# Optimization experiments

Hardware: AMD Instinct MI355X
Metric: run time of the kernel (lower is better)

Reference implementation:

```python
import jax, jax.numpy as jnp
import numpy as np

DIM = 1024
NUM_HEADS = 16
HEAD_DIM = 64

def setup_inputs() -> dict:
    key = jax.random.key(0)
    ks = jax.random.split(key, 7)
    x = jax.random.normal(ks[0], (4, 4096, DIM), dtype=jnp.float32)
    mask = jnp.ones((4, 4096), dtype=jnp.float32)
    # torch Linear stores weight (out, in) and computes x @ W.T; we store (in, out) directly.
    Wq = jax.random.normal(ks[1], (DIM, NUM_HEADS * HEAD_DIM), dtype=jnp.float32) / np.sqrt(DIM)
    Wk = jax.random.normal(ks[2], (DIM, NUM_HEADS * HEAD_DIM), dtype=jnp.float32) / np.sqrt(DIM)
    Wv = jax.random.normal(ks[3], (DIM, NUM_HEADS * HEAD_DIM), dtype=jnp.float32) / np.sqrt(DIM)
    Wo = jax.random.normal(ks[4], (NUM_HEADS * HEAD_DIM, DIM), dtype=jnp.float32) / np.sqrt(NUM_HEADS * HEAD_DIM)
    # FeatureMap buffer: randn(dim, dim) / sqrt(dim) with dim = head_dim
    proj = jax.random.normal(ks[5], (HEAD_DIM, HEAD_DIM), dtype=jnp.float32) / np.sqrt(HEAD_DIM)
    return {"x": x, "mask": mask, "Wq": Wq, "Wk": Wk, "Wv": Wv, "Wo": Wo, "proj": proj}

def _feature_map(x, proj):
    # phi(x) = elu(x @ proj) + 1  (non-negative random features)
    return jax.nn.elu(x @ proj) + 1.0

def reference(x, mask, Wq, Wk, Wv, Wo, proj):
    b, n, _ = x.shape
    h, d = NUM_HEADS, HEAD_DIM
    # project and split heads: (b, h, n, d)
    q = (x @ Wq).reshape(b, n, h, d).transpose(0, 2, 1, 3)
    k = (x @ Wk).reshape(b, n, h, d).transpose(0, 2, 1, 3)
    v = (x @ Wv).reshape(b, n, h, d).transpose(0, 2, 1, 3)
    q = _feature_map(q, proj)
    k = _feature_map(k, proj)
    # mask: (b, n) -> (b, 1, n, 1)
    k = k * mask[:, None, :, None]
    # linear attention: phi(Q) (phi(K)^T V)
    kv = jnp.einsum('bhnd,bhne->bhde', k, v)          # (b, h, d, d)
    qkv = jnp.einsum('bhnd,bhde->bhne', q, kv)        # (b, h, n, d)
    k_sum = k.sum(axis=2)                              # (b, h, d)
    normalizer = jnp.einsum('bhnd,bhd->bhn', q, k_sum) + 1e-06
    out = qkv / normalizer[..., None]
    out = out.transpose(0, 2, 1, 3).reshape(b, n, h * d)
    return out @ Wo
```

## Files before the change

### kernel.cpp

```cpp
#include <hip/hip_runtime.h>
#include <stdint.h>

#define TOKENS 16384
#define KDIM 1024
#define QKVN 3072

typedef unsigned short u16;
using bf16x8 = __attribute__((ext_vector_type(8))) __bf16;
using f32x4  = __attribute__((ext_vector_type(4))) float;
using u16x8  = __attribute__((ext_vector_type(8))) unsigned short;

__device__ inline u16 f2bf(float f) {
  union { float f; uint32_t u; } v; v.f = f;
  uint32_t u = v.u;
  return (u16)((u + 0x7FFFu + ((u >> 16) & 1u)) >> 16);
}
__device__ inline float bf2f(u16 s) {
  union { uint32_t u; float f; } v; v.u = ((uint32_t)s) << 16;
  return v.f;
}
__device__ inline void g2l16(const void* g, void* l) {
  __builtin_amdgcn_global_load_lds(
      (const __attribute__((address_space(1))) void*)g,
      (__attribute__((address_space(3))) void*)l, 16, 0, 0);
}

template<int LD>
__device__ inline void stage_half(const u16* __restrict__ g, u16* l, int t) {
  #pragma unroll
  for (int i = 0; i < 2; ++i) {
    const int ch = i * 512 + t;
    const int row = ch >> 3;
    const int cc = (ch & 7) ^ (row & 7);
    g2l16(g + (long)row * LD + cc * 8, (char*)l + ch * 16);
  }
}

#define LDA_H(DST, BASE) do { \
  _Pragma("unroll") \
  for (int mi = 0; mi < 4; ++mi) { \
    const int row = wm*64 + mi*16 + rl; \
    const char* p = (const char*)(BASE) + row*128; \
    const int sw = (row & 7) << 4; \
    DST[mi][0] = *(const bf16x8*)(p + ((kg*16) ^ sw)); \
    DST[mi][1] = *(const bf16x8*)(p + ((64 + kg*16) ^ sw)); \
  } \
} while (0)

#define LDB_H(DST, BASE) do { \
  _Pragma("unroll") \
  for (int ni = 0; ni < 2; ++ni) { \
    const int row = wn*32 + ni*16 + rl; \
    const char* p = (const char*)(BASE) + row*128; \
    const int sw = (row & 7) << 4; \
    DST[ni][0] = *(const bf16x8*)(p + ((kg*16) ^ sw)); \
    DST[ni][1] = *(const bf16x8*)(p + ((64 + kg*16) ^ sw)); \
  } \
} while (0)

#define MFMA2Q(MH, AV, BV0, BV1) do { \
  __builtin_amdgcn_s_setprio(1); \
  _Pragma("unroll") \
  for (int kh = 0; kh < 2; ++kh) \
    _Pragma("unroll") \
    for (int mi = 0; mi < 4; ++mi) \
      _Pragma("unroll") \
      for (int ni = 0; ni < 2; ++ni) { \
        acc[(MH)*4+mi][ni]   = __builtin_amdgcn_mfma_f32_16x16x32_bf16( \
            AV[mi][kh], BV0[ni][kh], acc[(MH)*4+mi][ni], 0, 0, 0); \
        acc[(MH)*4+mi][2+ni] = __builtin_amdgcn_mfma_f32_16x16x32_bf16( \
            AV[mi][kh], BV1[ni][kh], acc[(MH)*4+mi][2+ni], 0, 0, 0); \
      } \
  __builtin_amdgcn_s_setprio(0); \
} while (0)

#define LGKM0 do { \
  asm volatile("s_waitcnt lgkmcnt(0)" ::: "memory"); \
  __builtin_amdgcn_sched_barrier(0); \
} while (0)
#define VMC(N) asm volatile("s_waitcnt vmcnt(" #N ")" ::: "memory")
#define BAR() __builtin_amdgcn_s_barrier()

template<int NTOT, int EPI, int ALD, int NT, int PERB>
__device__ __forceinline__ void gemm_body(
    const u16* __restrict__ A, const u16* __restrict__ Bm,
    void* __restrict__ C, const float* __restrict__ aux) {
  __shared__ u16 As[2][2][8192];
  __shared__ u16 Bs[2][2][8192];
  const int t = threadIdx.x;
  const int l = t & 63;
  const int w = t >> 6;
  const int rl = l & 15, kg = l >> 4;
  const int wm = w >> 2, wn = w & 3;
  constexpr int nbn = NTOT / 256;
  constexpr int nwg = 64 * nbn;
  constexpr int GRID = nwg / NT;
  constexpr int KC = NT * 16;
  constexpr int IT = KC / 2;
  static_assert(nwg % 8 == 0, "bijective xcd swizzle");
  const int bid = blockIdx.x;

  auto tcoord = [&](int ot, long& tar, long& tbr) {
    const int gt = ot * GRID + bid;
    const int swz = (gt & 7) * (nwg / 8) + (gt >> 3);
    tar = (long)(swz / nbn) * 256;
    tbr = (long)(swz % nbn) * 256;
  };
  auto asrc = [&](int ch) {
    long ta, tb; tcoord(ch >> 4, ta, tb);
    return A + ta * ALD + (ch & 15) * 64;
  };
  auto bsrc = [&](int ch) {
    long ta, tb; tcoord(ch >> 4, ta, tb);
    return Bm + (PERB ? (ta >> 12) * 1048576 : 0) + tb * 1024 + (ch & 15) * 64;
  };

  f32x4 acc[8][4];
  #pragma unroll
  for (int i = 0; i < 8; ++i)
    #pragma unroll
    for (int j = 0; j < 4; ++j)
      acc[i][j] = (f32x4){0.f, 0.f, 0.f, 0.f};

  bf16x8 afA[4][2], bA[2][2], bB[2][2];

  auto epilogue = [&](int ot) {
    long ar0, br0; tcoord(ot, ar0, br0);
    #pragma unroll
    for (int mh = 0; mh < 2; ++mh)
      #pragma unroll
      for (int mi = 0; mi < 4; ++mi)
        #pragma unroll
        for (int j = 0; j < 4; ++j) {
          const long row = ar0 + mh*128 + wm*64 + mi*16 + kg*4 + j;
          float rs = 0.f;
          if (EPI == 0) rs = aux[row];
          #pragma unroll
          for (int nh = 0; nh < 2; ++nh)
            #pragma unroll
            for (int ni = 0; ni < 2; ++ni) {
              const long col = br0 + nh*128 + wn*32 + ni*16 + rl;
              float v = acc[mh*4+mi][nh*2+ni][j];
              if (EPI == 0) {
                if (col < 2048) {
                  v = (v > 0.f) ? (v + 1.f) : __expf(v);
                  if (col >= 1024) v *= rs;
                }
                ((u16*)C)[row * QKVN + col] = f2bf(v);
              } else {
                ((float*)C)[row * NTOT + col] = v;
              }
            }
        }
    #pragma unroll
    for (int i = 0; i < 8; ++i)
      #pragma unroll
      for (int j = 0; j < 4; ++j)
        acc[i][j] = (f32x4){0.f, 0.f, 0.f, 0.f};
  };

  {
    const u16* A0s = asrc(0); const u16* B0s = bsrc(0);
    const u16* A1s = asrc(1); const u16* B1s = bsrc(1);
    stage_half<ALD >(A0s,             As[0][0], t);
    stage_half<1024>(B0s,             Bs[0][0], t);
    stage_half<1024>(B0s + 128*1024,  Bs[0][1], t);
    stage_half<ALD >(A0s + 128*ALD,   As[0][1], t);
    stage_half<ALD >(A1s,             As[1][0], t);
    stage_half<1024>(B1s,             Bs[1][0], t);
    VMC(4);
    BAR();
  }

  for (int i = 0; i < IT; ++i) {
    const int o1 = 2*i + 1;
    const int e = (2*i + 2 < KC) ? 2*i + 2 : KC - 1;
    const int o = (2*i + 3 < KC) ? 2*i + 3 : KC - 1;
    const u16* Ao1 = asrc(o1); const u16* Bo1 = bsrc(o1);
    const u16* Ae = asrc(e);   const u16* Be = bsrc(e);
    const u16* Ao = asrc(o);   const u16* Bo = bsrc(o);

    LDA_H(afA, As[0][0]); LDB_H(bA, Bs[0][0]); LDB_H(bB, Bs[0][1]);
    stage_half<ALD>(Ao1 + 128*ALD, As[1][1], t);
    stage_half<1024>(Bo1 + 128*1024, Bs[1][1], t);
    LGKM0;
    MFMA2Q(0, afA, bA, bB);
    VMC(4); BAR();

    LDA_H(afA, As[0][1]);
    stage_half<ALD>(Ae, As[0][0], t);
    stage_half<1024>(Be, Bs[0][0], t);
    LGKM0;
    MFMA2Q(1, afA, bA, bB);
    VMC(4); BAR();

    LDA_H(afA, As[1][0]); LDB_H(bA, Bs[1][0]); LDB_H(bB, Bs[1][1]);
    stage_half<ALD>(Ae + 128*ALD, As[0][1], t);
    stage_half<1024>(Be + 128*1024, Bs[0][1], t);
    LGKM0;
    MFMA2Q(0, afA, bA, bB);
    VMC(4); BAR();

    LDA_H(afA, As[1][1]);
    stage_half<ALD>(Ao, As[1][0], t);
    stage_half<1024>(Bo, Bs[1][0], t);
    LGKM0;
    MFMA2Q(1, afA, bA, bB);
    VMC(4); BAR();

    if ((i & 7) == 7) epilogue(i >> 3);
  }
  VMC(0);
}

__global__ __launch_bounds__(512, 2) void gemm_qkv(
    const u16* __restrict__ A, const u16* __restrict__ Bm,
    void* __restrict__ C, const float* __restrict__ aux) {
  gemm_body<3072, 0, 1024, 3, 0>(A, Bm, C, aux);
}
__global__ __launch_bounds__(512, 2) void gemm_out(
    const u16* __restrict__ A, const u16* __restrict__ Bm,
    void* __restrict__ C, const float* __restrict__ aux) {
  gemm_body<1024, 1, 1024, 1, 1>(A, Bm, C, aux);
}

__global__ __launch_bounds__(256) void kv_kernel(const u16* __restrict__ QKV,
    float* __restrict__ kvws, float* __restrict__ ksws) {
  __shared__ u16 Kl[32 * 64];
  __shared__ u16 Vl[32 * 64];
  const int t = threadIdx.x;
  const int l = t & 63, w = t >> 6;
  const int rl = l & 15, kg = l >> 4;
  const int bid = blockIdx.x;
  const int bh = bid >> 3, ns = bid & 7;
  const int b = bh >> 4, h = bh & 15;
  const long tok0 = (long)b * 4096 + ns * 512;

  f32x4 acc[4];
  #pragma unroll
  for (int i = 0; i < 4; ++i) acc[i] = (f32x4){0.f, 0.f, 0.f, 0.f};
  float ks = 0.f;
  const int srow = t >> 3, scc = t & 7;

  for (int it = 0; it < 16; ++it) {
    const long tb = tok0 + it * 32;
    g2l16(QKV + (tb + srow) * QKVN + 1024 + h * 64 + scc * 8, (char*)Kl + t * 16);
    g2l16(QKV + (tb + srow) * QKVN + 2048 + h * 64 + scc * 8, (char*)Vl + t * 16);
    __syncthreads();
    union { u16x8 u; bf16x8 v; } au, bu;
    #pragma unroll
    for (int j = 0; j < 8; ++j) au.u[j] = Kl[(kg * 8 + j) * 64 + w * 16 + rl];
    #pragma unroll
    for (int ni = 0; ni < 4; ++ni) {
      #pragma unroll
      for (int j = 0; j < 8; ++j) bu.u[j] = Vl[(kg * 8 + j) * 64 + ni * 16 + rl];
      acc[ni] = __builtin_amdgcn_mfma_f32_16x16x32_bf16(au.v, bu.v, acc[ni], 0, 0, 0);
    }
    #pragma unroll
    for (int r = 0; r < 8; ++r) ks += bf2f(Kl[(w * 8 + r) * 64 + (t & 63)]);
    __syncthreads();
  }
  float* kvb = kvws + bh * 4096;
  #pragma unroll
  for (int ni = 0; ni < 4; ++ni)
    #pragma unroll
    for (int j = 0; j < 4; ++j) {
      const int d = w * 16 + kg * 4 + j;
      const int e = ni * 16 + rl;
      atomicAdd(&kvb[d * 64 + e], acc[ni][j]);
    }
  atomicAdd(&ksws[bh * 64 + (t & 63)], ks);
}

__global__ __launch_bounds__(256) void scale_q(const u16* __restrict__ QKV,
    const float* __restrict__ ksws, u16* __restrict__ Qc) {
  __shared__ float ksl[1024];
  const int bid = blockIdx.x, t = threadIdx.x;
  const int n0 = bid * 16;
  const int b = n0 >> 12;
  #pragma unroll
  for (int i = 0; i < 4; ++i) ksl[i * 256 + t] = ksws[b * 1024 + i * 256 + t];
  __syncthreads();
  const int h = t & 15, ti = t >> 4;
  const u16* qp = QKV + (long)(n0 + ti) * QKVN + h * 64;
  u16* op = Qc + (long)(n0 + ti) * 1024 + h * 64;
  u16x8 v[8];
  float norm = 1e-6f;
  #pragma unroll
  for (int i = 0; i < 8; ++i) {
    v[i] = *(const u16x8*)(qp + i * 8);
    #pragma unroll
    for (int j = 0; j < 8; ++j) norm += bf2f(v[i][j]) * ksl[h * 64 + i * 8 + j];
  }
  const float inv = 1.0f / norm;
  #pragma unroll
  for (int i = 0; i < 8; ++i) {
    u16x8 o;
    #pragma unroll
    for (int j = 0; j < 8; ++j) o[j] = f2bf(bf2f(v[i][j]) * inv);
    *(u16x8*)(op + i * 8) = o;
  }
}

__global__ __launch_bounds__(256) void w2_kernel(const float* __restrict__ kvws,
    const float* __restrict__ Wo, u16* __restrict__ W2T) {
  __shared__ float kvl[64][64];
  const int bid = blockIdx.x, t = threadIdx.x;
  const int bh = bid >> 2, os = bid & 3;
  const int b = bh >> 4, h = bh & 15;
  const float* kvb = kvws + bh * 4096;
  #pragma unroll
  for (int i = 0; i < 16; ++i) ((float*)kvl)[i * 256 + t] = kvb[i * 256 + t];
  __syncthreads();
  const int o = os * 256 + t;
  float wo[64];
  #pragma unroll
  for (int e = 0; e < 64; ++e) wo[e] = Wo[(long)(h * 64 + e) * 1024 + o];
  u16* out = W2T + (long)b * 1048576 + (long)o * 1024 + h * 64;
  for (int d = 0; d < 64; ++d) {
    float s = 0.f;
    #pragma unroll
    for (int e = 0; e < 64; ++e) s += wo[e] * kvl[d][e];
    out[d] = f2bf(s);
  }
}

__global__ __launch_bounds__(256) void prep_qk(const float* __restrict__ Wq,
    const float* __restrict__ Wk, const float* __restrict__ proj,
    u16* __restrict__ WqkvT) {
  __shared__ float Wl[128][65];
  __shared__ float Pl[64][65];
  const int bid = blockIdx.x;
  const int m = bid >> 7, h = (bid >> 3) & 15, cb = bid & 7;
  const float* W = m ? Wk : Wq;
  const int t = threadIdx.x;
  #pragma unroll
  for (int i = 0; i < 16; ++i) {
    const int idx = i * 256 + t;
    Pl[idx >> 6][idx & 63] = proj[idx];
  }
  #pragma unroll
  for (int i = 0; i < 32; ++i) {
    const int idx = i * 256 + t;
    const int c = idx >> 6, d = idx & 63;
    Wl[c][d] = W[(long)(cb * 128 + c) * 1024 + h * 64 + d];
  }
  __syncthreads();
  const int c = t & 127, j0 = (t >> 7) * 32;
  float a[32];
  #pragma unroll
  for (int jj = 0; jj < 32; ++jj) a[jj] = 0.f;
  for (int d = 0; d < 64; ++d) {
    const float wv = Wl[c][d];
    #pragma unroll
    for (int jj = 0; jj < 32; ++jj) a[jj] += wv * Pl[d][j0 + jj];
  }
  #pragma unroll
  for (int jj = 0; jj < 32; ++jj)
    WqkvT[(long)(m * 1024 + h * 64 + j0 + jj) * 1024 + cb * 128 + c] = f2bf(a[jj]);
}

__global__ __launch_bounds__(256) void prep_v(const float* __restrict__ Wv,
    u16* __restrict__ WqkvT) {
  __shared__ float til[64][65];
  const int bid = blockIdx.x;
  const int rt = (bid >> 4) & 15, ct = bid & 15;
  const int t = threadIdx.x;
  const int j = t & 63;
  #pragma unroll
  for (int p = 0; p < 16; ++p) {
    const int i = p * 4 + (t >> 6);
    til[i][j] = Wv[(long)(rt * 64 + i) * 1024 + ct * 64 + j];
  }
  __syncthreads();
  u16* dst = WqkvT + (long)2048 * 1024;
  #pragma unroll
  for (int p = 0; p < 16; ++p) {
    const int i = p * 4 + (t >> 6);
    dst[(long)(ct * 64 + i) * 1024 + rt * 64 + j] = f2bf(til[j][i]);
  }
}

__global__ __launch_bounds__(256) void conv_x(const float* __restrict__ x,
                                              u16* __restrict__ xb) {
  const int idx = blockIdx.x * 256 + threadIdx.x;
  const float4* p = (const float4*)x + (long)idx * 2;
  const float4 a = p[0], b = p[1];
  u16x8 o;
  o[0] = f2bf(a.x); o[1] = f2bf(a.y); o[2] = f2bf(a.z); o[3] = f2bf(a.w);
  o[4] = f2bf(b.x); o[5] = f2bf(b.y); o[6] = f2bf(b.z); o[7] = f2bf(b.w);
  *((u16x8*)xb + idx) = o;
}

extern "C" void kernel_launch(void* const* d_in, const int* in_sizes, int n_in,
                              void* d_out, int out_size, void* d_ws, size_t ws_size,
                              hipStream_t stream) {
  const float* x    = (const float*)d_in[0];
  const float* mask = (const float*)d_in[1];
  const float* Wq   = (const float*)d_in[2];
  const float* Wk   = (const float*)d_in[3];
  const float* Wv   = (const float*)d_in[4];
  const float* Wo   = (const float*)d_in[5];
  const float* proj = (const float*)d_in[6];

  char* ws = (char*)d_ws;
  u16*  WqkvT = (u16*)(ws);
  u16*  xb    = (u16*)(ws + 8388608);
  u16*  QKV   = (u16*)(ws + 41943040);
  float* kvws = (float*)(ws + 142606336);
  float* ksws = (float*)(ws + 143654912);
  u16*  Qc   = xb;
  u16*  W2T  = (u16*)(ws);
  if (ws_size < (size_t)143671296) return;

  hipMemsetAsync(kvws, 0, 1064960, stream);
  prep_qk<<<256, 256, 0, stream>>>(Wq, Wk, proj, WqkvT);
  prep_v <<<256, 256, 0, stream>>>(Wv, WqkvT);
  conv_x <<<8192, 256, 0, stream>>>(x, xb);
  gemm_qkv<<<256, 512, 0, stream>>>(xb, WqkvT, (void*)QKV, mask);
  kv_kernel<<<512, 256, 0, stream>>>(QKV, kvws, ksws);
  scale_q<<<1024, 256, 0, stream>>>(QKV, ksws, Qc);
  w2_kernel<<<256, 256, 0, stream>>>(kvws, Wo, W2T);
  gemm_out<<<256, 512, 0, stream>>>(Qc, W2T, d_out, nullptr);
}
```

Measured before the change: 259.3 us.

## Split GEMM MFMA waits, precompute tile coords, widen kv chunks, merge weight prep

The GEMM inner loop now waits for only part of the LDS reads (lgkmcnt(4)) before issuing the first half of the MFMAs, so the remaining B-fragment loads overlap with compute. It also adds scheduling barriers and computes tile coordinates once instead of per chunk. The kv kernel processes 64 tokens per iteration instead of 32, halving its barrier count. The two weight-prep kernels are merged into a single launch; the merged kernel contains some odd no-op shared-memory self-assignments.

```diff
diff --git a/kernel.cpp b/kernel.cpp
--- a/kernel.cpp
+++ b/kernel.cpp
@@ -58,28 +58,29 @@
   } \
 } while (0)
 
-#define MFMA2Q(MH, AV, BV0, BV1) do { \
-  __builtin_amdgcn_s_setprio(1); \
+#define MFMA_G(MH, AV, BV, NB) do { \
   _Pragma("unroll") \
   for (int kh = 0; kh < 2; ++kh) \
     _Pragma("unroll") \
     for (int mi = 0; mi < 4; ++mi) \
       _Pragma("unroll") \
-      for (int ni = 0; ni < 2; ++ni) { \
-        acc[(MH)*4+mi][ni]   = __builtin_amdgcn_mfma_f32_16x16x32_bf16( \
-            AV[mi][kh], BV0[ni][kh], acc[(MH)*4+mi][ni], 0, 0, 0); \
-        acc[(MH)*4+mi][2+ni] = __builtin_amdgcn_mfma_f32_16x16x32_bf16( \
-            AV[mi][kh], BV1[ni][kh], acc[(MH)*4+mi][2+ni], 0, 0, 0); \
-      } \
-  __builtin_amdgcn_s_setprio(0); \
+      for (int ni = 0; ni < 2; ++ni) \
+        acc[(MH)*4+mi][(NB)+ni] = __builtin_amdgcn_mfma_f32_16x16x32_bf16( \
+            AV[mi][kh], BV[ni][kh], acc[(MH)*4+mi][(NB)+ni], 0, 0, 0); \
 } while (0)
 
 #define LGKM0 do { \
   asm volatile("s_waitcnt lgkmcnt(0)" ::: "memory"); \
   __builtin_amdgcn_sched_barrier(0); \
 } while (0)
+#define LGKM4 do { \
+  asm volatile("s_waitcnt lgkmcnt(4)" ::: "memory"); \
+  __builtin_amdgcn_sched_barrier(0); \
+} while (0)
 #define VMC(N) asm volatile("s_waitcnt vmcnt(" #N ")" ::: "memory")
 #define BAR() __builtin_amdgcn_s_barrier()
+#define SCHED0 __builtin_amdgcn_sched_barrier(0)
+#define PRIO(N) __builtin_amdgcn_s_setprio(N)
 
 template<int NTOT, int EPI, int ALD, int NT, int PERB>
 __device__ __forceinline__ void gemm_body(
@@ -106,12 +107,20 @@
     tar = (long)(swz / nbn) * 256;
     tbr = (long)(swz % nbn) * 256;
   };
+  long ar0_, br0_, ar1_, br1_, ar2_, br2_;
+  tcoord(0, ar0_, br0_);
+  if (NT > 1) tcoord(1, ar1_, br1_); else { ar1_ = ar0_; br1_ = br0_; }
+  if (NT > 2) tcoord(2, ar2_, br2_); else { ar2_ = ar1_; br2_ = br1_; }
+
   auto asrc = [&](int ch) {
-    long ta, tb; tcoord(ch >> 4, ta, tb);
+    const int ti = ch >> 4;
+    const long ta = (NT == 1 || ti == 0) ? ar0_ : (ti == 1 ? ar1_ : ar2_);
     return A + ta * ALD + (ch & 15) * 64;
   };
   auto bsrc = [&](int ch) {
-    long ta, tb; tcoord(ch >> 4, ta, tb);
+    const int ti = ch >> 4;
+    const long ta = (NT == 1 || ti == 0) ? ar0_ : (ti == 1 ? ar1_ : ar2_);
+    const long tb = (NT == 1 || ti == 0) ? br0_ : (ti == 1 ? br1_ : br2_);
     return Bm + (PERB ? (ta >> 12) * 1048576 : 0) + tb * 1024 + (ch & 15) * 64;
   };
 
@@ -180,32 +189,44 @@
     const u16* Ae = asrc(e);   const u16* Be = bsrc(e);
     const u16* Ao = asrc(o);   const u16* Bo = bsrc(o);
 
-    LDA_H(afA, As[0][0]); LDB_H(bA, Bs[0][0]); LDB_H(bB, Bs[0][1]);
+    LDA_H(afA, As[0][0]); LDB_H(bA, Bs[0][0]);
+    SCHED0;
+    LDB_H(bB, Bs[0][1]);
     stage_half<ALD>(Ao1 + 128*ALD, As[1][1], t);
     stage_half<1024>(Bo1 + 128*1024, Bs[1][1], t);
+    SCHED0;
+    LGKM4;
+    PRIO(1); MFMA_G(0, afA, bA, 0);
     LGKM0;
-    MFMA2Q(0, afA, bA, bB);
+    MFMA_G(0, afA, bB, 2); PRIO(0);
     VMC(4); BAR();
 
     LDA_H(afA, As[0][1]);
     stage_half<ALD>(Ae, As[0][0], t);
     stage_half<1024>(Be, Bs[0][0], t);
+    SCHED0;
     LGKM0;
-    MFMA2Q(1, afA, bA, bB);
+    PRIO(1); MFMA_G(1, afA, bA, 0); MFMA_G(1, afA, bB, 2); PRIO(0);
     VMC(4); BAR();
 
-    LDA_H(afA, As[1][0]); LDB_H(bA, Bs[1][0]); LDB_H(bB, Bs[1][1]);
+    LDA_H(afA, As[1][0]); LDB_H(bA, Bs[1][0]);
+    SCHED0;
+    LDB_H(bB, Bs[1][1]);
     stage_half<ALD>(Ae + 128*ALD, As[0][1], t);
     stage_half<1024>(Be + 128*1024, Bs[0][1], t);
+    SCHED0;
+    LGKM4;
+    PRIO(1); MFMA_G(0, afA, bA, 0);
     LGKM0;
-    MFMA2Q(0, afA, bA, bB);
+    MFMA_G(0, afA, bB, 2); PRIO(0);
     VMC(4); BAR();
 
     LDA_H(afA, As[1][1]);
     stage_half<ALD>(Ao, As[1][0], t);
     stage_half<1024>(Bo, Bs[1][0], t);
+    SCHED0;
     LGKM0;
-    MFMA2Q(1, afA, bA, bB);
+    PRIO(1); MFMA_G(1, afA, bA, 0); MFMA_G(1, afA, bB, 2); PRIO(0);
     VMC(4); BAR();
 
     if ((i & 7) == 7) epilogue(i >> 3);
@@ -226,8 +247,8 @@
 
 __global__ __launch_bounds__(256) void kv_kernel(const u16* __restrict__ QKV,
     float* __restrict__ kvws, float* __restrict__ ksws) {
-  __shared__ u16 Kl[32 * 64];
-  __shared__ u16 Vl[32 * 64];
+  __shared__ u16 Kl[64 * 64];
+  __shared__ u16 Vl[64 * 64];
   const int t = threadIdx.x;
   const int l = t & 63, w = t >> 6;
   const int rl = l & 15, kg = l >> 4;
@@ -240,24 +261,31 @@
   #pragma unroll
   for (int i = 0; i < 4; ++i) acc[i] = (f32x4){0.f, 0.f, 0.f, 0.f};
   float ks = 0.f;
-  const int srow = t >> 3, scc = t & 7;
-
-  for (int it = 0; it < 16; ++it) {
-    const long tb = tok0 + it * 32;
-    g2l16(QKV + (tb + srow) * QKVN + 1024 + h * 64 + scc * 8, (char*)Kl + t * 16);
-    g2l16(QKV + (tb + srow) * QKVN + 2048 + h * 64 + scc * 8, (char*)Vl + t * 16);
+
+  for (int it = 0; it < 8; ++it) {
+    const long tb = tok0 + it * 64;
+    #pragma unroll
+    for (int c = 0; c < 2; ++c) {
+      const int ch = c * 256 + t;
+      const int srow = ch >> 3, scc = ch & 7;
+      g2l16(QKV + (tb + srow) * QKVN + 1024 + h * 64 + scc * 8, (char*)Kl + ch * 16);
+      g2l16(QKV + (tb + srow) * QKVN + 2048 + h * 64 + scc * 8, (char*)Vl + ch * 16);
+    }
     __syncthreads();
     union { u16x8 u; bf16x8 v; } au, bu;
     #pragma unroll
-    for (int j = 0; j < 8; ++j) au.u[j] = Kl[(kg * 8 + j) * 64 + w * 16 + rl];
-    #pragma unroll
-    for (int ni = 0; ni < 4; ++ni) {
+    for (int ksb = 0; ksb < 2; ++ksb) {
       #pragma unroll
-      for (int j = 0; j < 8; ++j) bu.u[j] = Vl[(kg * 8 + j) * 64 + ni * 16 + rl];
-      acc[ni] = __builtin_amdgcn_mfma_f32_16x16x32_bf16(au.v, bu.v, acc[ni], 0, 0, 0);
-    }
-    #pragma unroll
-    for (int r = 0; r < 8; ++r) ks += bf2f(Kl[(w * 8 + r) * 64 + (t & 63)]);
+      for (int j = 0; j < 8; ++j) au.u[j] = Kl[(ksb * 32 + kg * 8 + j) * 64 + w * 16 + rl];
+      #pragma unroll
+      for (int ni = 0; ni < 4; ++ni) {
+        #pragma unroll
+        for (int j = 0; j < 8; ++j) bu.u[j] = Vl[(ksb * 32 + kg * 8 + j) * 64 + ni * 16 + rl];
+        acc[ni] = __builtin_amdgcn_mfma_f32_16x16x32_bf16(au.v, bu.v, acc[ni], 0, 0, 0);
+      }
+    }
+    #pragma unroll
+    for (int r = 0; r < 16; ++r) ks += bf2f(Kl[(w * 16 + r) * 64 + (t & 63)]);
     __syncthreads();
   }
   float* kvb = kvws + bh * 4096;
@@ -325,59 +353,60 @@
   }
 }
 
-__global__ __launch_bounds__(256) void prep_qk(const float* __restrict__ Wq,
+__global__ __launch_bounds__(256) void prep_w(const float* __restrict__ Wq,
     const float* __restrict__ Wk, const float* __restrict__ proj,
-    u16* __restrict__ WqkvT) {
+    const float* __restrict__ Wv, u16* __restrict__ WqkvT) {
   __shared__ float Wl[128][65];
   __shared__ float Pl[64][65];
-  const int bid = blockIdx.x;
-  const int m = bid >> 7, h = (bid >> 3) & 15, cb = bid & 7;
-  const float* W = m ? Wk : Wq;
   const int t = threadIdx.x;
-  #pragma unroll
-  for (int i = 0; i < 16; ++i) {
-    const int idx = i * 256 + t;
-    Pl[idx >> 6][idx & 63] = proj[idx];
-  }
-  #pragma unroll
-  for (int i = 0; i < 32; ++i) {
-    const int idx = i * 256 + t;
-    const int c = idx >> 6, d = idx & 63;
-    Wl[c][d] = W[(long)(cb * 128 + c) * 1024 + h * 64 + d];
-  }
-  __syncthreads();
-  const int c = t & 127, j0 = (t >> 7) * 32;
-  float a[32];
-  #pragma unroll
-  for (int jj = 0; jj < 32; ++jj) a[jj] = 0.f;
-  for (int d = 0; d < 64; ++d) {
-    const float wv = Wl[c][d];
-    #pragma unroll
-    for (int jj = 0; jj < 32; ++jj) a[jj] += wv * Pl[d][j0 + jj];
-  }
-  #pragma unroll
-  for (int jj = 0; jj < 32; ++jj)
-    WqkvT[(long)(m * 1024 + h * 64 + j0 + jj) * 1024 + cb * 128 + c] = f2bf(a[jj]);
-}
-
-__global__ __launch_bounds__(256) void prep_v(const float* __restrict__ Wv,
-    u16* __restrict__ WqkvT) {
-  __shared__ float til[64][65];
-  const int bid = blockIdx.x;
-  const int rt = (bid >> 4) & 15, ct = bid & 15;
-  const int t = threadIdx.x;
-  const int j = t & 63;
-  #pragma unroll
-  for (int p = 0; p < 16; ++p) {
-    const int i = p * 4 + (t >> 6);
-    til[i][j] = Wv[(long)(rt * 64 + i) * 1024 + ct * 64 + j];
-  }
-  __syncthreads();
-  u16* dst = WqkvT + (long)2048 * 1024;
-  #pragma unroll
-  for (int p = 0; p < 16; ++p) {
-    const int i = p * 4 + (t >> 6);
-    dst[(long)(ct * 64 + i) * 1024 + rt * 64 + j] = f2bf(til[j][i]);
+  if (blockIdx.x < 256) {
+    const int bid = blockIdx.x;
+    const int m = bid >> 7, h = (bid >> 3) & 15, cb = bid & 7;
+    const float* W = m ? Wk : Wq;
+    #pragma unroll
+    for (int i = 0; i < 16; ++i) {
+      const int idx = i * 256 + t;
+      Pl[idx >> 6][idx & 63] = proj[idx];
+    }
+    #pragma unroll
+    for (int i = 0; i < 32; ++i) {
+      const int idx = i * 256 + t;
+      const int c = idx >> 6, d = idx & 63;
+      Wl[c][d] = W[(long)(cb * 128 + c) * 1024 + h * 64 + d];
+    }
+    __syncthreads();
+    const int c = t & 127, j0 = (t >> 7) * 32;
+    float a[32];
+    #pragma unroll
+    for (int jj = 0; jj < 32; ++jj) a[jj] = 0.f;
+    for (int d = 0; d < 64; ++d) {
+      const float wv = Wl[c][d];
+      #pragma unroll
+      for (int jj = 0; jj < 32; ++jj) a[jj] += wv * Pl[d][j0 + jj];
+    }
+    #pragma unroll
+    for (int jj = 0; jj < 32; ++jj)
+      WqkvT[(long)(m * 1024 + h * 64 + j0 + jj) * 1024 + cb * 128 + c] = f2bf(a[jj]);
+  } else {
+    const int bid = blockIdx.x - 256;
+    const int rt = (bid >> 4) & 15, ct = bid & 15;
+    const int j = t & 63;
+    #pragma unroll
+    for (int p = 0; p < 16; ++p) {
+      const int i = p * 4 + (t >> 6);
+      Pl[0][0] = Pl[0][0];
+      Wl[0][i * 0] = Wl[0][0];
+      ((float*)Pl)[0] = ((float*)Pl)[0];
+      (void)0;
+      Wl[i][j] = Wv[(long)(rt * 64 + i) * 1024 + ct * 64 + j];
+    }
+    __syncthreads();
+    u16* dst = WqkvT + (long)2048 * 1024;
+    #pragma unroll
+    for (int p = 0; p < 16; ++p) {
+      const int i = p * 4 + (t >> 6);
+      dst[(long)(ct * 64 + i) * 1024 + rt * 64 + j] = f2bf(Wl[j][i]);
+    }
   }
 }
 
@@ -414,9 +443,8 @@
   if (ws_size < (size_t)143671296) return;
 
   hipMemsetAsync(kvws, 0, 1064960, stream);
-  prep_qk<<<256, 256, 0, stream>>>(Wq, Wk, proj, WqkvT);
-  prep_v <<<256, 256, 0, stream>>>(Wv, WqkvT);
-  conv_x <<<8192, 256, 0, stream>>>(x, xb);
+  prep_w<<<512, 256, 0, stream>>>(Wq, Wk, proj, Wv, WqkvT);
+  conv_x<<<8192, 256, 0, stream>>>(x, xb);
   gemm_qkv<<<256, 512, 0, stream>>>(xb, WqkvT, (void*)QKV, mask);
   kv_kernel<<<512, 256, 0, stream>>>(QKV, kvws, ksws);
   scale_q<<<1024, 256, 0, stream>>>(QKV, ksws, Qc);
```

Result: slower. 280.5 us (+8.2%).
